# Performance work log

Measured on AMD Instinct MI355X. Metric: run time of the kernel, lower is better.

## Reference

```python
import jax, jax.numpy as jnp
import numpy as np

EPS = 1.1920929e-07  # torch F.rms_norm default eps = finfo(float32).eps
H = 8        # num_heads
KVH = 8      # num_kv_heads (must equal dim/head_dim for the view to be valid)
ROPE_BASE = 10000.0


def setup_inputs() -> dict:
    key = jax.random.key(0)
    ks = jax.random.split(key, 10)
    B, S, D, R = 2, 2048, 1024, 64
    x = jax.random.normal(ks[0], (B, S, D), jnp.float32)
    # scale the shared basis so the reconstructed matmul has ~unit-variance output
    basis_A = jax.random.normal(ks[1], (D, R), jnp.float32) / jnp.sqrt(jnp.float32(D))
    basis_B = jax.random.normal(ks[2], (R, D), jnp.float32) / jnp.sqrt(jnp.float32(R))
    mk_c = lambda k: 1.0 + 0.1 * jax.random.normal(k, (R,), jnp.float32)  # init is ones; perturb so q/k/v differ
    return {
        'x': x,
        'basis_A': basis_A,
        'basis_B': basis_B,
        'C_q': mk_c(ks[3]), 'C_k': mk_c(ks[4]), 'C_v': mk_c(ks[5]),
        'C_o': mk_c(ks[6]), 'C_fc': mk_c(ks[7]), 'C_proj': mk_c(ks[8]),
        'scale1': jnp.ones((D,), jnp.float32),
        'scale2': jnp.ones((D,), jnp.float32),
    }


def reference(x, basis_A, basis_B, C_q, C_k, C_v, C_o, C_fc, C_proj, scale1, scale2):
    B, S, D = x.shape
    HD = D // H          # head_dim = 128
    half = HD // 2

    def rms(h, s):
        return h * jax.lax.rsqrt(jnp.mean(h * h, axis=-1, keepdims=True) + EPS) * s

    def blin(h, C):  # BasisLinear: (h @ A) * C @ B
        return ((h @ basis_A) * C) @ basis_B

    # ---- attention sub-block ----
    n1 = rms(x, scale1)
    q = blin(n1, C_q).reshape(B, S, H, HD).transpose(0, 2, 1, 3)    # (B,H,S,HD)
    k = blin(n1, C_k).reshape(B, S, KVH, HD).transpose(0, 2, 1, 3)  # (B,KVH,S,HD)
    v = blin(n1, C_v).reshape(B, S, KVH, HD).transpose(0, 2, 1, 3)

    inv_freq = 1.0 / (ROPE_BASE ** (jnp.arange(0, HD, 2, dtype=jnp.float32) / HD))
    freqs = jnp.outer(jnp.arange(S, dtype=jnp.float32), inv_freq)   # (S, half)
    cos = jnp.cos(freqs)[None, None]                                # (1,1,S,half)
    sin = jnp.sin(freqs)[None, None]

    def rope(u):
        u1, u2 = u[..., :half], u[..., half:]
        return jnp.concatenate([u1 * cos + u2 * sin, -u1 * sin + u2 * cos], axis=-1)

    q = rope(q)
    k = rope(k)

    scores = jnp.einsum('bhqd,bhkd->bhqk', q, k) * (1.0 / jnp.sqrt(jnp.float32(HD)))
    causal = jnp.tril(jnp.ones((S, S), dtype=bool))
    scores = jnp.where(causal, scores, jnp.finfo(scores.dtype).min)
    attn = jax.nn.softmax(scores, axis=-1)
    y = jnp.einsum('bhqk,bhkd->bhqd', attn, v)
    y = y.transpose(0, 2, 1, 3).reshape(B, S, D)
    x = x + blin(y, C_o)

    # ---- MLP sub-block (SiLU, same width due to shared basis) ----
    n2 = rms(x, scale2)
    m = jax.nn.silu(blin(n2, C_fc))
    return x + blin(m, C_proj)
```

## Files before the change

kernel.cpp:

```cpp
#include <hip/hip_runtime.h>


#define Bn 2
#define Sn 2048
#define Dn 1024
#define Rn 64
#define Hn 8
#define HDn 128
#define Mn (Bn*Sn)
#define TSTRIDE ((size_t)Mn * Rn)

typedef __bf16 bf16x8 __attribute__((ext_vector_type(8)));
typedef float f32x4 __attribute__((ext_vector_type(4)));
typedef __attribute__((address_space(1))) const unsigned int g_u32;
typedef __attribute__((address_space(3))) unsigned int l_u32;

__device__ __forceinline__ float bf2f(unsigned short u){
    union { unsigned int i; float f; } x; x.i = ((unsigned int)u) << 16; return x.f;
}
__device__ __forceinline__ unsigned short f2bf(float f){
    union { float f; unsigned int i; } x; x.f = f;
    unsigned int r = x.i + 0x7fffu + ((x.i >> 16) & 1u);
    return (unsigned short)(r >> 16);
}
__device__ __forceinline__ unsigned int pk2(float a, float b){
    unsigned int r;
    asm("v_cvt_pk_bf16_f32 %0, %1, %2" : "=v"(r) : "v"(a), "v"(b));
    return r;
}
__device__ __forceinline__ float vexp2(float x){
    float r;
    asm("v_exp_f32 %0, %1" : "=v"(r) : "v"(x));
    return r;
}
__device__ __forceinline__ void gld16(const void* g, void* l){
    __builtin_amdgcn_global_load_lds((g_u32*)g, (l_u32*)l, 16, 0, 0);
}
__device__ __forceinline__ void dma32k(const char* src, char* dst, int tid){
    #pragma unroll
    for (int p = 0; p < 8; ++p)
        gld16(src + p * 4096 + tid * 16, dst + p * 4096 + tid * 16);
}
__device__ __forceinline__ float bflo(unsigned int u){
    union { unsigned int i; float f; } x; x.i = u << 16; return x.f;
}
__device__ __forceinline__ float bfhi(unsigned int u){
    union { unsigned int i; float f; } x; x.i = u & 0xffff0000u; return x.f;
}
__device__ __forceinline__ uint4 comb8(uint4 A, uint4 C, float Wc){
    uint4 r;
    unsigned int* a = (unsigned int*)&A;
    unsigned int* c = (unsigned int*)&C;
    unsigned int* o = (unsigned int*)&r;
    #pragma unroll
    for (int e = 0; e < 4; ++e){
        float lo = (bflo(a[e]) + bflo(c[e])) * Wc;
        float hi = (bfhi(a[e]) + bfhi(c[e])) * Wc;
        o[e] = pk2(lo, hi);
    }
    return r;
}

__global__ __launch_bounds__(256) void prep_g(const float* __restrict__ A,
                                              const float* __restrict__ Bsrc,
                                              const float* __restrict__ Cq, const float* __restrict__ Ck,
                                              const float* __restrict__ Cv, const float* __restrict__ Co,
                                              const float* __restrict__ Cfc, const float* __restrict__ Cpr,
                                              const float* __restrict__ s1, const float* __restrict__ s2,
                                              char* __restrict__ AtI1c, char* __restrict__ AtI0c,
                                              char* __restrict__ AtI2u, char* __restrict__ AtI0u,
                                              char* __restrict__ BIq, char* __restrict__ BIk,
                                              char* __restrict__ BIv, char* __restrict__ BIo,
                                              char* __restrict__ BIfc, char* __restrict__ BIpr,
                                              float2* __restrict__ rt){
    int idx = blockIdx.x * 256 + threadIdx.x;
    if (idx < 4 * 65536){
        int v = idx >> 16, e = idx & 65535;
        int r = e & 63, d = e >> 6;
        float sc = (v == 0) ? s1[d] : (v == 2) ? s2[d] : 1.f;
        unsigned short val = f2bf(A[d * 64 + r] * sc);
        if (v < 2){
            int us = (d >> 6) * 4096 + r * 64 + (((((d >> 3) & 7) << 4) ^ ((r & 7) << 4)) >> 1) + (d & 7);
            ((unsigned short*)(v == 0 ? AtI1c : AtI0c))[us] = val;
        } else {
            int us = (d >> 8) * 16384 + r * 256 + (((((d >> 3) & 31) << 4) ^ ((r & 7) << 4)) >> 1) + (d & 7);
            ((unsigned short*)(v == 2 ? AtI2u : AtI0u))[us] = val;
        }
    } else if (idx < 10 * 65536){
        int v = (idx >> 16) - 4, e = idx & 65535;
        int d = e & 1023, r = e >> 10;
        const float* C = v==0?Cq : v==1?Ck : v==2?Cv : v==3?Co : v==4?Cfc : Cpr;
        float extra = (v == 0) ? (0.08838834764831845f * 1.4426950408889634f) : 1.f;
        unsigned short val = f2bf(Bsrc[r * 1024 + d] * C[r] * extra);
        int us = (d >> 8) * 16384 + (d & 255) * 64 + ((((r >> 3) << 4) ^ ((d & 7) << 4)) >> 1) + (r & 7);
        ((unsigned short*)(v==0?BIq : v==1?BIk : v==2?BIv : v==3?BIo : v==4?BIfc : BIpr))[us] = val;
    } else if (idx < 10 * 65536 + Sn * 64){
        int e = idx - 10 * 65536;
        int s = e >> 6, f = e & 63;
        float inv = exp2f(-(float)f * (13.287712379549449f / 64.0f));
        float fr = (float)s * inv;
        float sn, cs; sincosf(fr, &sn, &cs);
        rt[e] = make_float2(cs, sn);
    }
}

__global__ __launch_bounds__(256) void down_g(const float* __restrict__ inp,
                                              const char* __restrict__ AtImg,
                                              unsigned short* __restrict__ tpart,
                                              float* __restrict__ sspart){
    __shared__ char xt[32768];
    __shared__ char at[32768];
    int tid = threadIdx.x;
    int m0 = blockIdx.x * 64, sp = blockIdx.y;
    int row = tid >> 2, q4 = tid & 3;
    int w = tid >> 6, lane = tid & 63, l4 = lane >> 4, lm = lane & 15;
    int swz = (row & 7) << 4;
    dma32k(AtImg + (size_t)sp * 32768, at, tid);
    float ss = 0.f;
    f32x4 acc[4];
    #pragma unroll
    for (int nt = 0; nt < 4; ++nt) acc[nt] = (f32x4){0.f,0.f,0.f,0.f};

    float4 xr[4];
    #define LOADX(c) { int k0 = sp * 256 + (c) * 64; \
        const float4* s = (const float4*)(inp + (size_t)(m0+row)*1024 + k0 + q4*16); \
        xr[0]=s[0]; xr[1]=s[1]; xr[2]=s[2]; xr[3]=s[3]; }

    LOADX(0);
    for (int c = 0; c < 4; ++c){
        char* xc = xt + c * 8192;
        #pragma unroll
        for (int i = 0; i < 4; ++i)
            ss += xr[i].x*xr[i].x + xr[i].y*xr[i].y + xr[i].z*xr[i].z + xr[i].w*xr[i].w;
        uint4 p0 = {pk2(xr[0].x,xr[0].y), pk2(xr[0].z,xr[0].w), pk2(xr[1].x,xr[1].y), pk2(xr[1].z,xr[1].w)};
        uint4 p1 = {pk2(xr[2].x,xr[2].y), pk2(xr[2].z,xr[2].w), pk2(xr[3].x,xr[3].y), pk2(xr[3].z,xr[3].w)};
        *(uint4*)(xc + row * 128 + ((q4 * 32) ^ swz)) = p0;
        *(uint4*)(xc + row * 128 + ((q4 * 32 + 16) ^ swz)) = p1;
        __syncthreads();
        if (c < 3) LOADX(c + 1);
        #pragma unroll
        for (int ks = 0; ks < 2; ++ks){
            int arow = 16 * w + lm;
            bf16x8 af = *(const bf16x8*)(xc + arow * 128 + ((ks*64 + l4*16) ^ ((arow & 7) << 4)));
            #pragma unroll
            for (int nt = 0; nt < 4; ++nt){
                int brow = nt * 16 + lm;
                bf16x8 bf = *(const bf16x8*)(at + c * 8192 + brow * 128 + ((ks*64 + l4*16) ^ ((brow & 7) << 4)));
                acc[nt] = __builtin_amdgcn_mfma_f32_16x16x32_bf16(af, bf, acc[nt], 0, 0, 0);
            }
        }
    }
    #undef LOADX
    ss += __shfl_xor(ss, 1); ss += __shfl_xor(ss, 2);
    if (q4 == 0) sspart[sp * Mn + m0 + row] = ss;
    #pragma unroll
    for (int nt = 0; nt < 4; ++nt)
        #pragma unroll
        for (int r = 0; r < 4; ++r){
            int ml = 16 * w + 4 * l4 + r;
            tpart[(size_t)sp * TSTRIDE + (size_t)(m0 + ml) * 64 + nt * 16 + lm] = f2bf(acc[nt][r]);
        }
}

__global__ __launch_bounds__(256) void downy_g(const unsigned short* __restrict__ ybf,
                                               const unsigned short* __restrict__ pab,
                                               const float* __restrict__ pl,
                                               const char* __restrict__ AtImg,
                                               unsigned short* __restrict__ tpart){
    __shared__ char xt[32768];
    __shared__ char at[32768];
    int tid = threadIdx.x;
    int m0 = blockIdx.x * 64, sp = blockIdx.y;
    int row = tid >> 2, q4 = tid & 3;
    int w = tid >> 6, lane = tid & 63, l4 = lane >> 4, lm = lane & 15;
    int swz = (row & 7) << 4;
    int jq = (m0 & (Sn - 1)) >> 7;
    int bpos = m0 >> 11;
    int srow = (m0 & 127) + row;
    dma32k(AtImg + (size_t)sp * 32768, at, tid);
    f32x4 acc[4];
    #pragma unroll
    for (int nt = 0; nt < 4; ++nt) acc[nt] = (f32x4){0.f,0.f,0.f,0.f};

    #define MFMAC(c) { \
        _Pragma("unroll") \
        for (int ks = 0; ks < 2; ++ks){ \
            int arow = 16 * w + lm; \
            bf16x8 af = *(const bf16x8*)(xt + (c) * 8192 + arow * 128 + ((ks*64 + l4*16) ^ ((arow & 7) << 4))); \
            _Pragma("unroll") \
            for (int nt = 0; nt < 4; ++nt){ \
                int brow = nt * 16 + lm; \
                bf16x8 bf = *(const bf16x8*)(at + (c) * 8192 + brow * 128 + ((ks*64 + l4*16) ^ ((brow & 7) << 4))); \
                acc[nt] = __builtin_amdgcn_mfma_f32_16x16x32_bf16(af, bf, acc[nt], 0, 0, 0); \
            } \
        } }

    if (jq < 8){
        const char* yb = (const char*)ybf;
        #pragma unroll
        for (int p = 0; p < 8; ++p){
            int c = p >> 1;
            int rw = (p & 1) * 32 + (tid >> 3);
            int gp = (tid & 7) ^ (rw & 7);
            gld16(yb + (size_t)(m0 + rw) * 2048 + sp * 512 + c * 128 + gp * 16,
                  xt + p * 4096 + tid * 16);
        }
        __syncthreads();
        for (int c = 0; c < 4; ++c) MFMAC(c);
    } else {
        uint4 xrb[2];
        #define LOADCMB(c) { int k0 = sp * 256 + (c) * 64; \
            int h = k0 >> 7; int d0 = k0 & 127; \
            int s0sl = (((bpos * 8 + h) * 8) + (jq - 8)) * 2; \
            const unsigned short* p0 = pab + (size_t)s0sl * 16384 + srow * 128 + d0 + q4 * 16; \
            const unsigned short* p1 = p0 + 16384; \
            float Wc = 1.f / (pl[s0sl * 128 + srow] + pl[(s0sl + 1) * 128 + srow]); \
            uint4 A0 = ((const uint4*)p0)[0], A1 = ((const uint4*)p0)[1]; \
            uint4 C0 = ((const uint4*)p1)[0], C1 = ((const uint4*)p1)[1]; \
            xrb[0] = comb8(A0, C0, Wc); xrb[1] = comb8(A1, C1, Wc); }
        LOADCMB(0);
        for (int c = 0; c < 4; ++c){
            char* xc = xt + c * 8192;
            *(uint4*)(xc + row * 128 + ((q4 * 32) ^ swz)) = xrb[0];
            *(uint4*)(xc + row * 128 + ((q4 * 32 + 16) ^ swz)) = xrb[1];
            __syncthreads();
            if (c < 3) LOADCMB(c + 1);
            MFMAC(c);
        }
        #undef LOADCMB
    }
    #undef MFMAC
    #pragma unroll
    for (int nt = 0; nt < 4; ++nt)
        #pragma unroll
        for (int r = 0; r < 4; ++r){
            int ml = 16 * w + 4 * l4 + r;
            tpart[(size_t)sp * TSTRIDE + (size_t)(m0 + ml) * 64 + nt * 16 + lm] = f2bf(acc[nt][r]);
        }
}

template<int DORMS>
__device__ __forceinline__ void stage_t(char* tt, const unsigned short* __restrict__ tpart,
                                        const float* __restrict__ sspart, int m0, int tid){
    int row = tid >> 2, q4 = tid & 3;
    const unsigned short* bp = tpart + (size_t)(m0 + row) * 64 + q4 * 16;
    float s[16];
    #pragma unroll
    for (int half = 0; half < 2; ++half){
        uint4 u0 = ((const uint4*)(bp + 0 * TSTRIDE))[half];
        uint4 u1 = ((const uint4*)(bp + 1 * TSTRIDE))[half];
        uint4 u2 = ((const uint4*)(bp + 2 * TSTRIDE))[half];
        uint4 u3 = ((const uint4*)(bp + 3 * TSTRIDE))[half];
        const unsigned int* a0 = (const unsigned int*)&u0;
        const unsigned int* a1 = (const unsigned int*)&u1;
        const unsigned int* a2 = (const unsigned int*)&u2;
        const unsigned int* a3 = (const unsigned int*)&u3;
        #pragma unroll
        for (int e = 0; e < 4; ++e){
            s[half*8 + 2*e]     = bflo(a0[e]) + bflo(a1[e]) + bflo(a2[e]) + bflo(a3[e]);
            s[half*8 + 2*e + 1] = bfhi(a0[e]) + bfhi(a1[e]) + bfhi(a2[e]) + bfhi(a3[e]);
        }
    }
    float rr = 1.f;
    if (DORMS){
        int m = m0 + row;
        float ssum = sspart[m] + sspart[Mn + m] + sspart[2*Mn + m] + sspart[3*Mn + m];
        rr = rsqrtf(ssum * (1.f / 1024.f) + 1.1920929e-07f);
    }
    #pragma unroll
    for (int i = 0; i < 16; ++i) s[i] *= rr;
    int swz = (row & 7) << 4;
    uint4 p0 = {pk2(s[0],s[1]), pk2(s[2],s[3]), pk2(s[4],s[5]), pk2(s[6],s[7])};
    uint4 p1 = {pk2(s[8],s[9]), pk2(s[10],s[11]), pk2(s[12],s[13]), pk2(s[14],s[15])};
    *(uint4*)(tt + row * 128 + ((q4 * 32) ^ swz)) = p0;
    *(uint4*)(tt + row * 128 + ((q4 * 32 + 16) ^ swz)) = p1;
}

template<int SILU, int HASBASE, int OUT_BF16, int DORMS, int BASEBF16>
__global__ __launch_bounds__(256) void up_g(const unsigned short* __restrict__ tpart,
                                            const float* __restrict__ sspart,
                                            const char* __restrict__ BtImg,
                                            const void* base,
                                            void* __restrict__ outp){
    __shared__ char tt[4096];
    __shared__ char bb[32768];
    int tid = threadIdx.x;
    int m0 = blockIdx.x * 32, n0 = blockIdx.y * 256;
    int w = tid >> 6, lane = tid & 63, l4 = lane >> 4, lm = lane & 15;
    int wm = w & 1, wn = w >> 1;
    dma32k(BtImg + (size_t)blockIdx.y * 32768, bb, tid);
    float bs[8][4];
    if (HASBASE){
        #pragma unroll
        for (int nt = 0; nt < 8; ++nt)
            #pragma unroll
            for (int r = 0; r < 4; ++r){
                int m = m0 + 16 * wm + 4 * l4 + r;
                int n = n0 + wn * 128 + nt * 16 + lm;
                bs[nt][r] = BASEBF16 ? bf2f(((const unsigned short*)base)[(size_t)m * 1024 + n])
                                     : ((const float*)base)[(size_t)m * 1024 + n];
            }
    }
    if (tid < 128) stage_t<DORMS>(tt, tpart, sspart, m0, tid);
    __syncthreads();
    bf16x8 af[2];
    #pragma unroll
    for (int ks = 0; ks < 2; ++ks){
        int arow = 16 * wm + lm;
        af[ks] = *(const bf16x8*)(tt + arow * 128 + ((ks*64 + l4*16) ^ ((arow & 7) << 4)));
    }
    f32x4 acc[8];
    #pragma unroll
    for (int nt = 0; nt < 8; ++nt) acc[nt] = (f32x4){0.f,0.f,0.f,0.f};
    #pragma unroll
    for (int nt = 0; nt < 8; ++nt){
        int brow = wn * 128 + nt * 16 + lm;
        #pragma unroll
        for (int ks = 0; ks < 2; ++ks){
            bf16x8 bf = *(const bf16x8*)(bb + brow * 128 + ((ks*64 + l4*16) ^ ((brow & 7) << 4)));
            acc[nt] = __builtin_amdgcn_mfma_f32_16x16x32_bf16(af[ks], bf, acc[nt], 0, 0, 0);
        }
    }
    #pragma unroll
    for (int nt = 0; nt < 8; ++nt)
        #pragma unroll
        for (int r = 0; r < 4; ++r){
            int m = m0 + 16 * wm + 4 * l4 + r;
            int n = n0 + wn * 128 + nt * 16 + lm;
            float v = acc[nt][r];
            if (SILU) v = v / (1.f + __expf(-v));
            if (HASBASE) v += bs[nt][r];
            if (OUT_BF16) ((unsigned short*)outp)[(size_t)m * 1024 + n] = f2bf(v);
            else          ((float*)outp)[(size_t)m * 1024 + n] = v;
        }
}

template<int SILU, int HASBASE, int STOREOUT, int SUMSQ, int DORMS_IN>
__global__ __launch_bounds__(256) void updown_g(const unsigned short* __restrict__ tpin,
                                                const float* __restrict__ sspin,
                                                const char* __restrict__ BtUimg,
                                                const char* __restrict__ AtDimg,
                                                const float* base,
                                                unsigned short* x1out,
                                                unsigned short* __restrict__ tpout,
                                                float* __restrict__ sspout){
    __shared__ char tt[4096];
    __shared__ char bb[32768];
    __shared__ char xb[16384];
    __shared__ float ssl[2][32];
    int tid = threadIdx.x;
    int m0 = blockIdx.x * 32, n0 = blockIdx.y * 256, sp = blockIdx.y;
    int w = tid >> 6, lane = tid & 63, l4 = lane >> 4, lm = lane & 15;
    int wm = w & 1, wn = w >> 1;
    dma32k(BtUimg + (size_t)sp * 32768, bb, tid);
    float bs[8][4];
    if (HASBASE){
        #pragma unroll
        for (int nt = 0; nt < 8; ++nt)
            #pragma unroll
            for (int r = 0; r < 4; ++r){
                int m = m0 + 16 * wm + 4 * l4 + r;
                int n = n0 + wn * 128 + nt * 16 + lm;
                bs[nt][r] = base[(size_t)m * 1024 + n];
            }
    }
    if (tid < 128) stage_t<DORMS_IN>(tt, tpin, sspin, m0, tid);
    __syncthreads();
    bf16x8 af[2];
    #pragma unroll
    for (int ks = 0; ks < 2; ++ks){
        int arow = 16 * wm + lm;
        af[ks] = *(const bf16x8*)(tt + arow * 128 + ((ks*64 + l4*16) ^ ((arow & 7) << 4)));
    }
    f32x4 acc[8];
    #pragma unroll
    for (int nt = 0; nt < 8; ++nt) acc[nt] = (f32x4){0.f,0.f,0.f,0.f};
    #pragma unroll
    for (int nt = 0; nt < 8; ++nt){
        int brow = wn * 128 + nt * 16 + lm;
        #pragma unroll
        for (int ks = 0; ks < 2; ++ks){
            bf16x8 bf = *(const bf16x8*)(bb + brow * 128 + ((ks*64 + l4*16) ^ ((brow & 7) << 4)));
            acc[nt] = __builtin_amdgcn_mfma_f32_16x16x32_bf16(af[ks], bf, acc[nt], 0, 0, 0);
        }
    }
    float val[8][4];
    float sq[4] = {0.f, 0.f, 0.f, 0.f};
    #pragma unroll
    for (int nt = 0; nt < 8; ++nt)
        #pragma unroll
        for (int r = 0; r < 4; ++r){
            int m = m0 + 16 * wm + 4 * l4 + r;
            int n = n0 + wn * 128 + nt * 16 + lm;
            float v = acc[nt][r];
            if (SILU) v = v / (1.f + __expf(-v));
            if (HASBASE) v += bs[nt][r];
            val[nt][r] = v;
            if (STOREOUT) x1out[(size_t)m * 1024 + n] = f2bf(v);
            if (SUMSQ) sq[r] += v * v;
        }
    if (SUMSQ){
        #pragma unroll
        for (int r = 0; r < 4; ++r){
            float s_ = sq[r];
            s_ += __shfl_xor(s_, 1);
            s_ += __shfl_xor(s_, 2);
            s_ += __shfl_xor(s_, 4);
            s_ += __shfl_xor(s_, 8);
            if (lm == 0) ssl[wn][16 * wm + 4 * l4 + r] = s_;
        }
    }
    __syncthreads();
    dma32k(AtDimg + (size_t)sp * 32768, bb, tid);
    #pragma unroll
    for (int nt = 0; nt < 8; ++nt)
        #pragma unroll
        for (int r = 0; r < 4; ++r){
            int mrow = 16 * wm + 4 * l4 + r;
            int cn = wn * 128 + nt * 16 + lm;
            *(unsigned short*)(xb + mrow * 512 + ((cn * 2) ^ ((mrow & 7) << 4))) = f2bf(val[nt][r]);
        }
    __syncthreads();
    if (SUMSQ && tid < 32)
        sspout[sp * Mn + m0 + tid] = ssl[0][tid] + ssl[1][tid];
    f32x4 acc2[2];
    acc2[0] = (f32x4){0.f,0.f,0.f,0.f};
    acc2[1] = (f32x4){0.f,0.f,0.f,0.f};
    #pragma unroll
    for (int kk = 0; kk < 8; ++kk){
        int arow = 16 * (w & 1) + lm;
        bf16x8 a2 = *(const bf16x8*)(xb + arow * 512 + ((kk * 64 + l4 * 16) ^ ((arow & 7) << 4)));
        #pragma unroll
        for (int j = 0; j < 2; ++j){
            int brow = (2 * (w >> 1) + j) * 16 + lm;
            bf16x8 b2 = *(const bf16x8*)(bb + brow * 512 + ((kk * 64 + l4 * 16) ^ ((brow & 7) << 4)));
            acc2[j] = __builtin_amdgcn_mfma_f32_16x16x32_bf16(a2, b2, acc2[j], 0, 0, 0);
        }
    }
    #pragma unroll
    for (int j = 0; j < 2; ++j)
        #pragma unroll
        for (int r = 0; r < 4; ++r){
            int ml = 16 * (w & 1) + 4 * l4 + r;
            int nc = (2 * (w >> 1) + j) * 16 + lm;
            tpout[(size_t)sp * TSTRIDE + (size_t)(m0 + ml) * 64 + nc] = f2bf(acc2[j][r]);
        }
}

__global__ __launch_bounds__(256) void qkv_g(const unsigned short* __restrict__ tpart,
                                             const float* __restrict__ sspart,
                                             const char* __restrict__ BIq,
                                             const char* __restrict__ BIk,
                                             const char* __restrict__ BIv,
                                             const float2* __restrict__ rt,
                                             unsigned short* __restrict__ qout,
                                             char* __restrict__ Kimg,
                                             char* __restrict__ Vimg){
    __shared__ char tt[8192];
    __shared__ char bb[32768];
    int tid = threadIdx.x;
    int m0 = blockIdx.x * 64, n0 = blockIdx.y * 256;
    int which = blockIdx.z;
    int b = m0 >> 11, s0 = m0 & (Sn - 1);
    int h0 = n0 >> 7;
    int w = tid >> 6, lane = tid & 63, l4 = lane >> 4, lm = lane & 15;
    const char* BI = (which == 0) ? BIq : (which == 1) ? BIk : BIv;
    dma32k(BI + (size_t)blockIdx.y * 32768, bb, tid);
    stage_t<1>(tt, tpart, sspart, m0, tid);
    __syncthreads();
    bf16x8 af[2];
    #pragma unroll
    for (int ks = 0; ks < 2; ++ks){
        int arow = 16 * w + lm;
        af[ks] = *(const bf16x8*)(tt + arow * 128 + ((ks*64 + l4*16) ^ ((arow & 7) << 4)));
    }
    f32x4 acc[16];
    #pragma unroll
    for (int nt = 0; nt < 16; ++nt) acc[nt] = (f32x4){0.f,0.f,0.f,0.f};
    #pragma unroll
    for (int nt = 0; nt < 16; ++nt){
        int brow = nt * 16 + lm;
        #pragma unroll
        for (int ks = 0; ks < 2; ++ks){
            bf16x8 bf = *(const bf16x8*)(bb + brow * 128 + ((ks*64 + l4*16) ^ ((brow & 7) << 4)));
            acc[nt] = __builtin_amdgcn_mfma_f32_16x16x32_bf16(af[ks], bf, acc[nt], 0, 0, 0);
        }
    }
    if (which < 2){
        float2 cs[4][4];
        #pragma unroll
        for (int ntb = 0; ntb < 4; ++ntb)
            #pragma unroll
            for (int r = 0; r < 4; ++r)
                cs[ntb][r] = rt[(size_t)(s0 + 16*w + 4*l4 + r) * 64 + ntb * 16 + lm];
        #pragma unroll
        for (int g = 0; g < 2; ++g)
            #pragma unroll
            for (int ntb = 0; ntb < 4; ++ntb){
                int lo = g*8 + ntb, hi = lo + 4;
                #pragma unroll
                for (int r = 0; r < 4; ++r){
                    float2 c = cs[ntb][r];
                    float a = acc[lo][r], bq = acc[hi][r];
                    acc[lo][r] = a * c.x + bq * c.y;
                    acc[hi][r] = -a * c.y + bq * c.x;
                }
            }
        __syncthreads();
        #pragma unroll
        for (int nt = 0; nt < 16; ++nt)
            #pragma unroll
            for (int r = 0; r < 4; ++r){
                int nl = nt * 16 + lm, ml2 = 16 * w + 4 * l4 + r;
                *(unsigned short*)(bb + ml2 * 512 + ((nl * 2) ^ ((ml2 & 7) << 4))) = f2bf(acc[nt][r]);
            }
        __syncthreads();
        if (which == 0){
            int ml = tid >> 2, seg = tid & 3;
            int head = h0 + (seg >> 1), hd0q = (seg & 1) * 64;
            size_t dstbase = (((size_t)(b * 8 + head) * Sn + (s0 + ml)) * 128 + hd0q);
            #pragma unroll
            for (int j = 0; j < 8; ++j){
                uint4 v = *(const uint4*)(bb + ml * 512 + ((seg * 128 + j * 16) ^ ((ml & 7) << 4)));
                *(uint4*)(qout + dstbase + j * 8) = v;
            }
        } else {
            int ml = tid >> 2, seg = tid & 3;
            int hd0q = (seg & 1) * 64;
            int head = h0 + (seg >> 1);
            int pr = 16 * (ml & 3) + (ml >> 2);
            size_t rowb = (((size_t)(b * 8 + head) * 32 + (s0 >> 6)) * 64 + pr) * 256;
            #pragma unroll
            for (int j = 0; j < 8; ++j){
                uint4 v = *(const uint4*)(bb + ml * 512 + ((seg * 128 + j * 16) ^ ((ml & 7) << 4)));
                int cb = hd0q * 2 + j * 16;
                *(uint4*)(Kimg + rowb + (cb ^ ((pr & 7) << 4))) = v;
            }
        }
    } else {
        __syncthreads();
        #pragma unroll
        for (int nt = 0; nt < 16; ++nt)
            #pragma unroll
            for (int r = 0; r < 4; ++r){
                int nl = nt * 16 + lm, ml2 = 16 * w + 4 * l4 + r;
                *(unsigned short*)(bb + nl * 128 + ((ml2 * 2) ^ ((nl & 7) << 4))) = f2bf(acc[nt][r]);
            }
        __syncthreads();
        int head = h0 + (tid >> 7), d = tid & 127;
        size_t rowb = (((size_t)(b * 8 + head) * 32 + (s0 >> 6)) * 128 + d) * 128;
        #pragma unroll
        for (int j = 0; j < 8; ++j){
            uint4 v = *(const uint4*)(bb + tid * 128 + ((j * 16) ^ ((tid & 7) << 4)));
            *(uint4*)(Vimg + rowb + ((j * 16) ^ ((d & 7) << 4))) = v;
        }
    }
}

__global__ __launch_bounds__(256, 2) void attn2_kernel(const unsigned short* __restrict__ qb,
                                                       const char* __restrict__ Kimg,
                                                       const char* __restrict__ Vimg,
                                                       unsigned short* __restrict__ ybf,
                                                       unsigned short* __restrict__ pab,
                                                       float* __restrict__ pl){
    __shared__ uint4 smem4[81920 / 16];
    char* smem = (char*)smem4;
    int tid = threadIdx.x;
    int w = tid >> 6, lane = tid & 63, l4 = lane >> 4, lm = lane & 15;
    int o = blockIdx.x;
    int bh, slot;
    if (o < 128){
        int cat = o >> 5;
        int k = o & 31;
        if (cat == 0){ bh = k & 15; slot = (k >> 4); }
        else { bh = k >> 1; slot = (k & 1) ? (8 + cat + 8) : (8 + cat); }
    } else if (o < 256){
        int k16 = 32 + (o - 128);
        bh = k16 & 15;
        int inst = k16 >> 4;
        slot = (inst < 9) ? inst : 16;
    } else {
        int cat = (o - 256) >> 5;
        int k = (o - 256) & 31;
        bh = k >> 1;
        int base = 15 - cat;
        slot = (k & 1) ? (base + 8) : base;
    }
    int grp = slot >> 3, g = slot & 7;
    int J, t0, niters, direct, slice;
    if (grp == 0){ J = 8 + g;  t0 = 0;  niters = 16;         direct = 0; slice = (bh * 8 + g) * 2; }
    else if (grp == 1){ J = 15 - g; t0 = 16; niters = 2 * J - 14; direct = 0; slice = (bh * 8 + (J - 8)) * 2 + 1; }
    else { J = 7 - g;  t0 = 0;  niters = 2 * J + 2;  direct = 1; slice = 0; }
    int b = bh >> 3, h = bh & 7;
    int qrow0w = 128 * J + 32 * w;
    int wqmax = qrow0w + 31;

    bf16x8 qf[2][4];
    #pragma unroll
    for (int f = 0; f < 2; ++f){
        const unsigned short* qg = qb + ((size_t)bh * Sn + qrow0w + 16 * f + lm) * HDn;
        #pragma unroll
        for (int df = 0; df < 4; ++df)
            qf[f][df] = *(const bf16x8*)(qg + df * 32 + l4 * 8);
    }
    f32x4 acc[2][8];
    #pragma unroll
    for (int f = 0; f < 2; ++f)
        #pragma unroll
        for (int dg = 0; dg < 8; ++dg) acc[f][dg] = (f32x4){0.f,0.f,0.f,0.f};
    float lp[2][4];
    #pragma unroll
    for (int f = 0; f < 2; ++f)
        #pragma unroll
        for (int r = 0; r < 4; ++r) lp[f][r] = 0.f;

    const float OFF = 11.541560327111708f;
    size_t imgbase = (size_t)bh * 32 * 16384;

    #define STAGE_DMA(T, BUFB) { size_t tb = imgbase + (size_t)(T) * 16384; \
        _Pragma("unroll") for (int i2 = 0; i2 < 4; ++i2){ \
            gld16(Kimg + tb + i2 * 4096 + tid * 16, smem + (BUFB) + i2 * 4096 + tid * 16); \
            gld16(Vimg + tb + i2 * 4096 + tid * 16, smem + (BUFB) + 16384 + i2 * 4096 + tid * 16); } }

    STAGE_DMA(t0, 0);
    __syncthreads();

    for (int it = 0; it < niters; ++it){
        int t = t0 + it;
        int bsel = (it & 1) << 15;
        if (it + 1 < niters)
            STAGE_DMA(t + 1, bsel ^ 32768);
        if (64 * t <= wqmax){
            char* KL = smem + bsel;
            char* VL = smem + bsel + 16384;
            char* pb = smem + 65536 + (w << 12);
            __builtin_amdgcn_s_setprio(1);
            f32x4 sf[2][4];
            #pragma unroll
            for (int kc = 0; kc < 4; ++kc){ sf[0][kc] = (f32x4){0.f,0.f,0.f,0.f}; sf[1][kc] = (f32x4){0.f,0.f,0.f,0.f}; }
            #pragma unroll
            for (int kc = 0; kc < 4; ++kc){
                int krow = 16 * kc + lm;
                int ksw = (krow & 7) << 4;
                #pragma unroll
                for (int df = 0; df < 4; ++df){
                    bf16x8 kf = *(const bf16x8*)(KL + krow * 256 + ((df * 64 + l4 * 16) ^ ksw));
                    sf[0][kc] = __builtin_amdgcn_mfma_f32_16x16x32_bf16(qf[0][df], kf, sf[0][kc], 0, 0, 0);
                    sf[1][kc] = __builtin_amdgcn_mfma_f32_16x16x32_bf16(qf[1][df], kf, sf[1][kc], 0, 0, 0);
                }
            }
            bf16x8 vf0[8];
            #pragma unroll
            for (int dg = 0; dg < 8; ++dg){
                int vrow = 16 * dg + lm;
                vf0[dg] = *(const bf16x8*)(VL + vrow * 128 + ((l4 * 16) ^ ((vrow & 7) << 4)));
            }
            bool needmask = (64 * t + 63 > qrow0w);
            #pragma unroll
            for (int f = 0; f < 2; ++f){
                #pragma unroll
                for (int r = 0; r < 4; ++r){
                    float s0v = sf[f][0][r], s1v = sf[f][1][r],
                          s2v = sf[f][2][r], s3v = sf[f][3][r];
                    if (needmask){
                        int qr = qrow0w + 16 * f + 4 * l4 + r;
                        int j0k = 64 * t + 4 * lm;
                        s0v = (j0k     > qr) ? -1e30f : s0v;
                        s1v = (j0k + 1 > qr) ? -1e30f : s1v;
                        s2v = (j0k + 2 > qr) ? -1e30f : s2v;
                        s3v = (j0k + 3 > qr) ? -1e30f : s3v;
                    }
                    float p0 = vexp2(s0v - OFF), p1 = vexp2(s1v - OFF),
                          p2 = vexp2(s2v - OFF), p3 = vexp2(s3v - OFF);
                    lp[f][r] += p0 + p1 + p2 + p3;
                    int prow = 16 * f + 4 * l4 + r;
                    uint2 pkd = {pk2(p0, p1), pk2(p2, p3)};
                    *(uint2*)(pb + prow * 128 + ((lm * 8) ^ ((prow & 7) << 4))) = pkd;
                }
            }
            {
                int pcol = (l4 * 16) ^ ((lm & 7) << 4);
                bf16x8 pa0 = *(const bf16x8*)(pb + lm * 128 + pcol);
                bf16x8 pa1 = *(const bf16x8*)(pb + (16 + lm) * 128 + pcol);
                #pragma unroll
                for (int dg = 0; dg < 8; ++dg){
                    acc[0][dg] = __builtin_amdgcn_mfma_f32_16x16x32_bf16(pa0, vf0[dg], acc[0][dg], 0, 0, 0);
                    acc[1][dg] = __builtin_amdgcn_mfma_f32_16x16x32_bf16(pa1, vf0[dg], acc[1][dg], 0, 0, 0);
                }
            }
            {
                int pcol = (64 + l4 * 16) ^ ((lm & 7) << 4);
                bf16x8 pa0 = *(const bf16x8*)(pb + lm * 128 + pcol);
                bf16x8 pa1 = *(const bf16x8*)(pb + (16 + lm) * 128 + pcol);
                #pragma unroll
                for (int dg = 0; dg < 8; ++dg){
                    int vrow = 16 * dg + lm;
                    bf16x8 vf = *(const bf16x8*)(VL + vrow * 128 + ((64 + l4 * 16) ^ ((vrow & 7) << 4)));
                    acc[0][dg] = __builtin_amdgcn_mfma_f32_16x16x32_bf16(pa0, vf, acc[0][dg], 0, 0, 0);
                    acc[1][dg] = __builtin_amdgcn_mfma_f32_16x16x32_bf16(pa1, vf, acc[1][dg], 0, 0, 0);
                }
            }
            __builtin_amdgcn_s_setprio(0);
        }
        __syncthreads();
    }
    #undef STAGE_DMA
    float lsum[2][4];
    #pragma unroll
    for (int f = 0; f < 2; ++f)
        #pragma unroll
        for (int r = 0; r < 4; ++r){
            float l_ = lp[f][r];
            l_ += __shfl_xor(l_, 1);
            l_ += __shfl_xor(l_, 2);
            l_ += __shfl_xor(l_, 4);
            l_ += __shfl_xor(l_, 8);
            lsum[f][r] = l_;
        }
    if (direct){
        #pragma unroll
        for (int f = 0; f < 2; ++f)
            #pragma unroll
            for (int r = 0; r < 4; ++r){
                float inv = 1.f / lsum[f][r];
                int row = qrow0w + 16 * f + 4 * l4 + r;
                unsigned short* yr = ybf + ((size_t)b * Sn + row) * Dn + h * HDn;
                #pragma unroll
                for (int dg = 0; dg < 8; ++dg)
                    yr[16 * dg + lm] = f2bf(acc[f][dg][r] * inv);
            }
    } else {
        unsigned short* pa_ = pab + (size_t)slice * 16384;
        #pragma unroll
        for (int f = 0; f < 2; ++f)
            #pragma unroll
            for (int r = 0; r < 4; ++r){
                int row = 32 * w + 16 * f + 4 * l4 + r;
                #pragma unroll
                for (int dg = 0; dg < 8; ++dg)
                    pa_[row * 128 + 16 * dg + lm] = f2bf(acc[f][dg][r]);
                if (lm == 0)
                    pl[slice * 128 + row] = lsum[f][r];
            }
    }
}

extern "C" void kernel_launch(void* const* d_in, const int* in_sizes, int n_in,
                              void* d_out, int out_size, void* d_ws, size_t ws_size,
                              hipStream_t stream){
    const float* x      = (const float*)d_in[0];
    const float* A      = (const float*)d_in[1];
    const float* Bm     = (const float*)d_in[2];
    const float* C_q    = (const float*)d_in[3];
    const float* C_k    = (const float*)d_in[4];
    const float* C_v    = (const float*)d_in[5];
    const float* C_o    = (const float*)d_in[6];
    const float* C_fc   = (const float*)d_in[7];
    const float* C_proj = (const float*)d_in[8];
    const float* scale1 = (const float*)d_in[9];
    const float* scale2 = (const float*)d_in[10];
    float* out = (float*)d_out;

    char* ws = (char*)d_ws;
    size_t off = 0;
    auto alloc = [&](size_t bytes)->char*{ char* p = ws + off; off += (bytes + 255) & ~(size_t)255; return p; };
    unsigned short* qb   = (unsigned short*)alloc((size_t)Mn * Dn * 2);
    char*           Kimg = alloc((size_t)16 * 32 * 16384);
    char*           Vimg = alloc((size_t)16 * 32 * 16384);
    unsigned short* ybf  = (unsigned short*)alloc((size_t)Mn * Dn * 2);
    unsigned short* pab  = (unsigned short*)alloc((size_t)256 * 16384 * 2);
    float*          pl   = (float*)alloc((size_t)256 * 128 * 4);
    unsigned short* tpA  = (unsigned short*)alloc(4 * TSTRIDE * 2);
    unsigned short* tpB  = (unsigned short*)alloc(4 * TSTRIDE * 2);
    unsigned short* x1b  = (unsigned short*)alloc((size_t)Mn * Dn * 2);
    float*          sspA = (float*)alloc(4 * (size_t)Mn * 4);
    float*          sspB = (float*)alloc(4 * (size_t)Mn * 4);
    char*           AtI1c = alloc(131072);
    char*           AtI0c = alloc(131072);
    char*           AtI2u = alloc(131072);
    char*           AtI0u = alloc(131072);
    char*           BIq   = alloc(131072);
    char*           BIk   = alloc(131072);
    char*           BIv   = alloc(131072);
    char*           BIo   = alloc(131072);
    char*           BIfc  = alloc(131072);
    char*           BIpr  = alloc(131072);
    float2*         rt    = (float2*)alloc((size_t)Sn * 64 * 8);

    prep_g<<<3072, 256, 0, stream>>>(A, Bm, C_q, C_k, C_v, C_o, C_fc, C_proj,
                                     scale1, scale2,
                                     AtI1c, AtI0c, AtI2u, AtI0u,
                                     BIq, BIk, BIv, BIo, BIfc, BIpr, rt);
    down_g<<<dim3(Mn / 64, 4), 256, 0, stream>>>(x, AtI1c, tpA, sspA);
    qkv_g<<<dim3(Mn / 64, 4, 3), 256, 0, stream>>>(tpA, sspA, BIq, BIk, BIv, rt, qb, Kimg, Vimg);
    attn2_kernel<<<384, 256, 0, stream>>>(qb, Kimg, Vimg, ybf, pab, pl);
    downy_g<<<dim3(Mn / 64, 4), 256, 0, stream>>>(ybf, pab, pl, AtI0c, tpA);
    updown_g<0, 1, 1, 1, 0><<<dim3(Mn / 32, 4), 256, 0, stream>>>(
        tpA, nullptr, BIo, AtI2u, x, x1b, tpB, sspB);
    updown_g<1, 0, 0, 0, 1><<<dim3(Mn / 32, 4), 256, 0, stream>>>(
        tpB, sspB, BIfc, AtI0u, nullptr, nullptr, tpA, nullptr);
    up_g<0, 1, 0, 0, 1><<<dim3(Mn / 32, 4), 256, 0, stream>>>(tpA, nullptr, BIpr, x1b, out);
}
```

Before: 92.52 us.

## Pair two query work-items per 512-thread attention block sharing K/V staging

The attention kernel now runs 192 blocks of 512 threads instead of 384 blocks of 256. Each half of the block handles a different query slot of the same batch-head, and slots are paired so both halves walk the same K/V tiles. Each staged K/V tile in shared memory is therefore reused by twice as many waves, halving global K/V traffic per unit of work. In exchange the block has more threads and shared memory, and one block per CU runs instead of two. Paired slots with fewer iterations sit idle while their partner finishes, and there are fewer blocks to balance across CUs.

```diff
diff --git a/kernel.cpp b/kernel.cpp
--- a/kernel.cpp
+++ b/kernel.cpp
@@ -557,42 +557,37 @@
     }
 }
 
-__global__ __launch_bounds__(256, 2) void attn2_kernel(const unsigned short* __restrict__ qb,
+__global__ __launch_bounds__(512, 1) void attn2_kernel(const unsigned short* __restrict__ qb,
                                                        const char* __restrict__ Kimg,
                                                        const char* __restrict__ Vimg,
                                                        unsigned short* __restrict__ ybf,
                                                        unsigned short* __restrict__ pab,
                                                        float* __restrict__ pl){
-    __shared__ uint4 smem4[81920 / 16];
+    __shared__ uint4 smem4[98304 / 16];
     char* smem = (char*)smem4;
     int tid = threadIdx.x;
-    int w = tid >> 6, lane = tid & 63, l4 = lane >> 4, lm = lane & 15;
+    int w = tid >> 6;
+    int sw = w & 3;
+    int sel = w >> 2;
+    int lane = tid & 63, l4 = lane >> 4, lm = lane & 15;
     int o = blockIdx.x;
-    int bh, slot;
-    if (o < 128){
-        int cat = o >> 5;
-        int k = o & 31;
-        if (cat == 0){ bh = k & 15; slot = (k >> 4); }
-        else { bh = k >> 1; slot = (k & 1) ? (8 + cat + 8) : (8 + cat); }
-    } else if (o < 256){
-        int k16 = 32 + (o - 128);
-        bh = k16 & 15;
-        int inst = k16 >> 4;
-        slot = (inst < 9) ? inst : 16;
+    int pc = o >> 4, bh = o & 15;
+    int slot, nit_blk;
+    if (pc < 8){
+        nit_blk = 16;
+        slot = sel ? (16 + pc) : pc;
     } else {
-        int cat = (o - 256) >> 5;
-        int k = (o - 256) & 31;
-        bh = k >> 1;
-        int base = 15 - cat;
-        slot = (k & 1) ? (base + 8) : base;
-    }
-    int grp = slot >> 3, g = slot & 7;
+        int g = pc - 8;
+        nit_blk = 16 - 2 * g;
+        slot = sel ? (15 - g) : (8 + g);
+    }
+    int grp = slot >> 3, g2 = slot & 7;
     int J, t0, niters, direct, slice;
-    if (grp == 0){ J = 8 + g;  t0 = 0;  niters = 16;         direct = 0; slice = (bh * 8 + g) * 2; }
-    else if (grp == 1){ J = 15 - g; t0 = 16; niters = 2 * J - 14; direct = 0; slice = (bh * 8 + (J - 8)) * 2 + 1; }
-    else { J = 7 - g;  t0 = 0;  niters = 2 * J + 2;  direct = 1; slice = 0; }
+    if (grp == 0){ J = 8 + g2;  t0 = 0;  niters = 16;         direct = 0; slice = (bh * 8 + g2) * 2; }
+    else if (grp == 1){ J = 15 - g2; t0 = 16; niters = 2 * J - 14; direct = 0; slice = (bh * 8 + (J - 8)) * 2 + 1; }
+    else { J = 7 - g2;  t0 = 0;  niters = 2 * J + 2;  direct = 1; slice = 0; }
     int b = bh >> 3, h = bh & 7;
-    int qrow0w = 128 * J + 32 * w;
+    int qrow0w = 128 * J + 32 * sw;
     int wqmax = qrow0w + 31;
 
     bf16x8 qf[2][4];
@@ -618,19 +613,19 @@
     size_t imgbase = (size_t)bh * 32 * 16384;
 
     #define STAGE_DMA(T, BUFB) { size_t tb = imgbase + (size_t)(T) * 16384; \
-        _Pragma("unroll") for (int i2 = 0; i2 < 4; ++i2){ \
-            gld16(Kimg + tb + i2 * 4096 + tid * 16, smem + (BUFB) + i2 * 4096 + tid * 16); \
-            gld16(Vimg + tb + i2 * 4096 + tid * 16, smem + (BUFB) + 16384 + i2 * 4096 + tid * 16); } }
+        _Pragma("unroll") for (int i2 = 0; i2 < 2; ++i2){ \
+            gld16(Kimg + tb + i2 * 8192 + tid * 16, smem + (BUFB) + i2 * 8192 + tid * 16); \
+            gld16(Vimg + tb + i2 * 8192 + tid * 16, smem + (BUFB) + 16384 + i2 * 8192 + tid * 16); } }
 
     STAGE_DMA(t0, 0);
     __syncthreads();
 
-    for (int it = 0; it < niters; ++it){
+    for (int it = 0; it < nit_blk; ++it){
         int t = t0 + it;
         int bsel = (it & 1) << 15;
-        if (it + 1 < niters)
+        if (it + 1 < nit_blk)
             STAGE_DMA(t + 1, bsel ^ 32768);
-        if (64 * t <= wqmax){
+        if (it < niters && 64 * t <= wqmax){
             char* KL = smem + bsel;
             char* VL = smem + bsel + 16384;
             char* pb = smem + 65536 + (w << 12);
@@ -735,7 +730,7 @@
         for (int f = 0; f < 2; ++f)
             #pragma unroll
             for (int r = 0; r < 4; ++r){
-                int row = 32 * w + 16 * f + 4 * l4 + r;
+                int row = 32 * sw + 16 * f + 4 * l4 + r;
                 #pragma unroll
                 for (int dg = 0; dg < 8; ++dg)
                     pa_[row * 128 + 16 * dg + lm] = f2bf(acc[f][dg][r]);
@@ -793,7 +788,7 @@
                                      BIq, BIk, BIv, BIo, BIfc, BIpr, rt);
     down_g<<<dim3(Mn / 64, 4), 256, 0, stream>>>(x, AtI1c, tpA, sspA);
     qkv_g<<<dim3(Mn / 64, 4, 3), 256, 0, stream>>>(tpA, sspA, BIq, BIk, BIv, rt, qb, Kimg, Vimg);
-    attn2_kernel<<<384, 256, 0, stream>>>(qb, Kimg, Vimg, ybf, pab, pl);
+    attn2_kernel<<<192, 512, 0, stream>>>(qb, Kimg, Vimg, ybf, pab, pl);
     downy_g<<<dim3(Mn / 64, 4), 256, 0, stream>>>(ybf, pab, pl, AtI0c, tpA);
     updown_g<0, 1, 1, 1, 0><<<dim3(Mn / 32, 4), 256, 0, stream>>>(
         tpA, nullptr, BIo, AtI2u, x, x1b, tpB, sspB);
```

Result: slower. 101.7 us (+9.9%).
